# Kernel tuning notes

Measured on AMD Instinct MI355X. Metric: run time of the kernel, lower is better.

## Reference

```python
import jax, jax.numpy as jnp
import numpy as np

# Config matching init_kwargs: dim=256, input_resolution=(64,64), num_heads=8,
# stride=2, dynamic_factor=2, window_size=8, Attention_Group=2, postype='rel', k=None
DIM, H, W = 256, 64, 64
HEADS, HG, STRIDE, WS, FACTOR = 8, 2, 2, 8, 2.0
GC = DIM // HG                 # channels per attention group (offset net width)
HC = DIM // HEADS              # per-head channels
RH, RW = H // STRIDE, W // STRIDE
WH, WW = H // WS, W // WS
B = 2
MLP_HID = 4 * DIM
EPS = 1e-5


def _grid_sample(img, grid):
    # img: (N, C, H, W); grid: (N, Hg, Wg, 2) with (row, col) in [-1, 1].
    # Bilinear, align_corners=True, zero padding (matches F.grid_sample).
    N, C, Hi, Wi = img.shape
    rows = (grid[..., 0] + 1.0) * 0.5 * (Hi - 1)
    cols = (grid[..., 1] + 1.0) * 0.5 * (Wi - 1)
    r0f = jnp.floor(rows); c0f = jnp.floor(cols)
    wr = rows - r0f; wc = cols - c0f
    r0 = r0f.astype(jnp.int32); c0 = c0f.astype(jnp.int32)

    def gather(ri, ci):
        valid = ((ri >= 0) & (ri < Hi) & (ci >= 0) & (ci < Wi)).astype(img.dtype)
        rc = jnp.clip(ri, 0, Hi - 1); cc = jnp.clip(ci, 0, Wi - 1)
        vals = jax.vmap(lambda im, r, c: im[:, r, c])(img, rc, cc)  # (N, C, Hg, Wg)
        return vals * valid[:, None]

    return (gather(r0, c0) * ((1 - wr) * (1 - wc))[:, None]
            + gather(r0, c0 + 1) * ((1 - wr) * wc)[:, None]
            + gather(r0 + 1, c0) * (wr * (1 - wc))[:, None]
            + gather(r0 + 1, c0 + 1) * (wr * wc)[:, None])


def _ln2d(z, g, b):
    mu = jnp.mean(z, axis=1, keepdims=True)
    var = jnp.var(z, axis=1, keepdims=True)
    return (z - mu) * jax.lax.rsqrt(var + EPS) * g[None, :, None, None] + b[None, :, None, None]


def _conv1x1(z, w, b=None):
    out = jnp.einsum('oc,bchw->bohw', w, z)
    return out if b is None else out + b[None, :, None, None]


def _forward(x, ln1_g, ln1_b, q_w, q_b, k_w, k_b, v_w, v_b,
             off1_w, off2_w, off3_w, bn_g, bn_b, bn_m, bn_v, off4_w,
             posembed, proj_w, proj_b, ln2_g, ln2_b,
             mlp_w1, mlp_b1, mlp_w2, mlp_b2):
    Bx, C = x.shape[0], x.shape[1]
    R, NW, WT = RH * RW, WH * WW, WS * WS
    scale = C ** -0.5  # original uses dim**-0.5 (not head_dim) as default qk scale

    xa = _ln2d(x, ln1_g, ln1_b)
    q = _conv1x1(xa, q_w, q_b)

    # ---- per-group offset prediction: 3 depthwise strided convs -> BN -> GELU -> 1x1 ----
    qg = q.reshape(Bx * HG, GC, H, W)

    def dw(z, w):
        return jax.lax.conv_general_dilated(z, w, (2, 2), ((1, 1), (1, 1)),
                feature_group_count=GC, dimension_numbers=('NCHW', 'OIHW', 'NCHW'))

    o = dw(dw(dw(qg, off1_w), off2_w), off3_w)  # (B*HG, GC, WH, WW)
    o = (o - bn_m[None, :, None, None]) * jax.lax.rsqrt(bn_v + EPS)[None, :, None, None]
    o = o * bn_g[None, :, None, None] + bn_b[None, :, None, None]
    o = jax.nn.gelu(o, approximate=False)
    off = jnp.einsum('oc,bchw->bohw', off4_w, o)               # (B*HG, 2R, WH, WW)
    off = off.reshape(Bx * HG, 2, R, NW).transpose(0, 3, 2, 1)  # (B*HG, NW, R, 2)
    ranges = jnp.array([1.0 / H, 1.0 / W], dtype=x.dtype)
    off = jnp.tanh(off) * ranges * FACTOR

    # ---- reference points normalized to [-1, 1] (align_corners=True convention) ----
    ref_r = (jnp.arange(RH, dtype=x.dtype) * STRIDE) / (H - 1) * 2.0 - 1.0
    ref_c = (jnp.arange(RW, dtype=x.dtype) * STRIDE) / (W - 1) * 2.0 - 1.0
    ref = jnp.stack(jnp.meshgrid(ref_r, ref_c, indexing='ij'), axis=-1).reshape(R, 2)
    grid = off + ref[None, None]                                # (B*HG, NW, R, 2)

    # ---- deformable gather of values at predicted sample locations ----
    value = xa.reshape(Bx * HG, GC, H, W)
    samp = _grid_sample(value, grid).reshape(Bx, C, NW, R)

    kk = _conv1x1(samp, k_w, k_b).reshape(Bx * HEADS, HC, NW, R).transpose(0, 2, 1, 3)
    vv = _conv1x1(samp, v_w, v_b).reshape(Bx * HEADS, HC, NW, R).transpose(0, 2, 1, 3)

    # ---- windowed queries ----
    wq = q.reshape(Bx * HEADS, HC, H, W).transpose(0, 2, 3, 1)
    wq = wq.reshape(Bx * HEADS, WH, WS, WW, WS, HC).transpose(0, 1, 3, 2, 4, 5)
    wq = wq.reshape(Bx * HEADS, NW, WT, HC) * scale

    attn = jnp.einsum('nwqc,nwcr->nwqr', wq, kk)                # (B*h, NW, WT, R)

    # ---- relative position bias: query pixel vs. (stride-spaced) reference point ----
    rel_y = (jnp.arange(RH) * STRIDE)[None, :] - jnp.arange(H)[:, None] + (H - 1)  # (H, RH)
    rel_x = (jnp.arange(RW) * STRIDE)[None, :] - jnp.arange(W)[:, None] + (W - 1)  # (W, RW)
    t = posembed[:, rel_y, :]                                   # (h, H, RH, 2W-1)
    bias = t[:, :, :, rel_x]                                    # (h, H, RH, W, RW)
    bias = bias.transpose(0, 1, 3, 2, 4).reshape(HEADS, H, W, R)
    bias = bias.reshape(HEADS, WH, WS, WW, WS, R).transpose(0, 1, 3, 2, 4, 5)
    bias = bias.reshape(HEADS, NW, WT, R)

    attn = attn.reshape(Bx, HEADS, NW, WT, R) + bias[None]
    attn = jax.nn.softmax(attn, axis=-1).reshape(Bx * HEADS, NW, WT, R)
    out = jnp.einsum('nwqr,nwcr->nwqc', attn, vv)               # (B*h, NW, WT, HC)
    out = out.reshape(Bx * HEADS, WH, WW, WS, WS, HC).transpose(0, 1, 3, 2, 4, 5)
    out = out.reshape(Bx, HEADS, H, W, HC).transpose(0, 1, 4, 2, 3).reshape(Bx, C, H, W)
    out = _conv1x1(out, proj_w, proj_b)

    x = x + out
    xm = _ln2d(x, ln2_g, ln2_b)
    hdn = jax.nn.gelu(_conv1x1(xm, mlp_w1, mlp_b1), approximate=False)
    return x + _conv1x1(hdn, mlp_w2, mlp_b2)


def setup_inputs() -> dict:
    key = jax.random.key(0)
    ks = jax.random.split(key, 16)
    f32 = jnp.float32

    def n(k, shape, std=0.02):
        return jax.random.normal(k, shape, dtype=f32) * std

    R = RH * RW
    return {
        'x': jax.random.normal(ks[0], (B, DIM, H, W), dtype=f32),
        'ln1_g': jnp.ones((DIM,), f32), 'ln1_b': jnp.zeros((DIM,), f32),
        'q_w': n(ks[1], (DIM, DIM)), 'q_b': jnp.zeros((DIM,), f32),
        'k_w': n(ks[2], (DIM, DIM)), 'k_b': jnp.zeros((DIM,), f32),
        'v_w': n(ks[3], (DIM, DIM)), 'v_b': jnp.zeros((DIM,), f32),
        'off1_w': n(ks[4], (GC, 1, 3, 3)),
        'off2_w': n(ks[5], (GC, 1, 3, 3)),
        'off3_w': n(ks[6], (GC, 1, 3, 3)),
        'bn_g': jnp.ones((GC,), f32), 'bn_b': jnp.zeros((GC,), f32),
        'bn_m': jnp.zeros((GC,), f32), 'bn_v': jnp.ones((GC,), f32),
        'off4_w': n(ks[7], (2 * R, GC)),
        'posembed': n(ks[8], (HEADS, 2 * H - 1, 2 * W - 1), std=0.01),
        'proj_w': n(ks[9], (DIM, DIM)), 'proj_b': jnp.zeros((DIM,), f32),
        'ln2_g': jnp.ones((DIM,), f32), 'ln2_b': jnp.zeros((DIM,), f32),
        'mlp_w1': n(ks[10], (MLP_HID, DIM)), 'mlp_b1': jnp.zeros((MLP_HID,), f32),
        'mlp_w2': n(ks[11], (DIM, MLP_HID)), 'mlp_b2': jnp.zeros((DIM,), f32),
    }


def reference(x, ln1_g, ln1_b, q_w, q_b, k_w, k_b, v_w, v_b,
              off1_w, off2_w, off3_w, bn_g, bn_b, bn_m, bn_v, off4_w,
              posembed, proj_w, proj_b, ln2_g, ln2_b,
              mlp_w1, mlp_b1, mlp_w2, mlp_b2):
    return _forward(x, ln1_g, ln1_b, q_w, q_b, k_w, k_b, v_w, v_b,
                    off1_w, off2_w, off3_w, bn_g, bn_b, bn_m, bn_v, off4_w,
                    posembed, proj_w, proj_b, ln2_g, ln2_b,
                    mlp_w1, mlp_b1, mlp_w2, mlp_b2)
```

## Files before the change

### kernel.cpp

```cpp
#include <hip/hip_runtime.h>
#include <hip/hip_bf16.h>
#include <math.h>


typedef __hip_bfloat16 bf16;
typedef __bf16 bf16x8 __attribute__((ext_vector_type(8)));
typedef float f32x4 __attribute__((ext_vector_type(4)));
typedef unsigned int u32x4 __attribute__((ext_vector_type(4)));

union U16x8 { uint4 u4; u32x4 v4; unsigned short us[8]; };

__device__ __forceinline__ float cvt(float x) { return x; }
__device__ __forceinline__ float cvt(bf16 x) { return __bfloat162float(x); }
__device__ __forceinline__ float b2f(unsigned short u) {
  union { float f; unsigned int v; } x; x.v = ((unsigned int)u) << 16; return x.f;
}
__device__ __forceinline__ unsigned short f2b(float f) {
  bf16 h = __float2bfloat16(f);
  return *reinterpret_cast<unsigned short*>(&h);
}
__device__ __forceinline__ float gelu_f(float x) {
  return 0.5f * x * (1.0f + erff(x * 0.7071067811865475f));
}
__device__ __forceinline__ void stout(float* p, float v) { *p = v; }
__device__ __forceinline__ void stout(bf16* p, float v) { *p = __float2bfloat16(v); }

__global__ __launch_bounds__(256) void setup_kernel(
    const float* __restrict__ x, const float* __restrict__ g,
    const float* __restrict__ bta,
    const float* __restrict__ q_w, const float* __restrict__ q_b,
    const float* __restrict__ k_w, const float* __restrict__ v_w,
    const float* __restrict__ pjw, const float* __restrict__ w1,
    const float* __restrict__ w2, const float* __restrict__ off4w,
    bf16* __restrict__ out, float* __restrict__ xnhwc,
    unsigned short* __restrict__ wqkv, float* __restrict__ bqkv,
    unsigned short* __restrict__ wproj, unsigned short* __restrict__ wmlp1,
    unsigned short* __restrict__ wmlp2, unsigned short* __restrict__ woff4i)
{
  __shared__ float s1[8][32], s2[8][32];
  __shared__ unsigned short tb[32][264];
  int bid = blockIdx.x;
  int t = threadIdx.x;
  if (bid < 256) {
    int pos = t & 31, cs = t >> 5;
    int p = bid * 32 + pos;
    int bb = p >> 12, hw = p & 4095;
    const float* xp = x + (size_t)bb * 256 * 4096 + hw;
    float vloc[32];
    float sum = 0.f, ss = 0.f;
#pragma unroll
    for (int i = 0; i < 32; ++i) {
      float v = xp[(size_t)(cs * 32 + i) * 4096];
      vloc[i] = v; sum += v; ss += v * v;
    }
    s1[cs][pos] = sum; s2[cs][pos] = ss;
    {
      float* xo = xnhwc + (size_t)p * 256 + cs * 32;
#pragma unroll
      for (int qd = 0; qd < 8; ++qd)
        *(float4*)(xo + qd * 4) = make_float4(vloc[qd*4], vloc[qd*4+1],
                                              vloc[qd*4+2], vloc[qd*4+3]);
    }
    __syncthreads();
    if (cs == 0) {
      float S = 0.f, Q = 0.f;
#pragma unroll
      for (int i = 0; i < 8; ++i) { S += s1[i][pos]; Q += s2[i][pos]; }
      float mu = S * (1.f / 256.f);
      float var = Q * (1.f / 256.f) - mu * mu;
      s1[0][pos] = mu;
      s2[0][pos] = rsqrtf(var + 1e-5f);
    }
    __syncthreads();
    float mu = s1[0][pos], rs = s2[0][pos];
#pragma unroll
    for (int i = 0; i < 32; ++i) {
      int c = cs * 32 + i;
      tb[pos][c] = f2b((vloc[i] - mu) * rs * g[c] + bta[c]);
    }
    __syncthreads();
    int px = t >> 3, grp = t & 7;
    bf16* op = out + ((size_t)bid * 32 + px) * 256 + grp * 32;
#pragma unroll
    for (int q = 0; q < 4; ++q)
      *(uint4*)(op + q * 8) = *(const uint4*)&tb[px][grp * 32 + q * 8];
  } else {
    int idx = (bid - 256) * 256 + t;
    const int S0 = 768 * 256;
    const int S1 = S0 + 768;
    const int S2 = S1 + 256 * 256;
    const int S3 = S2 + 1024 * 256;
    const int S4 = S3 + 256 * 1024;
    const int S5 = S4 + 2048 * 128;
    if (idx < S0) {
      int n = idx >> 8, c = idx & 255;
      float v;
      if (n < 256)       v = q_w[n * 256 + c];
      else if (n < 512)  v = k_w[(n - 256) * 256 + c];
      else               v = v_w[(n - 512) * 256 + c];
      wqkv[idx] = f2b(v);
    } else if (idx < S1) {
      int n = idx - S0;
      bqkv[n] = (n < 256) ? q_b[n] : 0.f;
    } else if (idx < S2) {
      wproj[idx - S1] = f2b(pjw[idx - S1]);
    } else if (idx < S3) {
      wmlp1[idx - S2] = f2b(w1[idx - S2]);
    } else if (idx < S4) {
      wmlp2[idx - S3] = f2b(w2[idx - S3]);
    } else if (idx < S5) {
      int kk = idx - S4;
      int n = kk >> 7, c = kk & 127;
      woff4i[kk] = f2b(off4w[((size_t)((n & 1) * 1024 + (n >> 1))) * 128 + c]);
    }
  }
}

__global__ __launch_bounds__(256) void ln2_kernel(
    const bf16* __restrict__ xin, const float* __restrict__ g,
    const float* __restrict__ bta, bf16* __restrict__ out)
{
  __shared__ float sa[8][32], sb[8][32];
  __shared__ float mu_s[32], rs_s[32];
  int t = threadIdx.x;
  int px = t >> 3, grp = t & 7;
  size_t p = (size_t)blockIdx.x * 32 + px;
  const bf16* xp = xin + p * 256 + grp * 32;
  float v[32]; float sum = 0.f, ss = 0.f;
#pragma unroll
  for (int q = 0; q < 4; ++q) {
    U16x8 u; u.u4 = *(const uint4*)(xp + q * 8);
#pragma unroll
    for (int j = 0; j < 8; ++j) {
      float f = b2f(u.us[j]); v[q * 8 + j] = f; sum += f; ss += f * f;
    }
  }
  sa[grp][px] = sum; sb[grp][px] = ss;
  __syncthreads();
  if (t < 32) {
    float S = 0.f, Q = 0.f;
#pragma unroll
    for (int i = 0; i < 8; ++i) { S += sa[i][t]; Q += sb[i][t]; }
    float mu = S * (1.f / 256.f);
    mu_s[t] = mu;
    rs_s[t] = rsqrtf(Q * (1.f / 256.f) - mu * mu + 1e-5f);
  }
  __syncthreads();
  float mu = mu_s[px], rs = rs_s[px];
  bf16* op = out + p * 256 + grp * 32;
#pragma unroll
  for (int q = 0; q < 4; ++q) {
    U16x8 o;
#pragma unroll
    for (int j = 0; j < 8; ++j) {
      int c = grp * 32 + q * 8 + j;
      o.us[j] = f2b((v[q * 8 + j] - mu) * rs * g[c] + bta[c]);
    }
    *(uint4*)(op + q * 8) = o.u4;
  }
}

template<int OUTM, int RESM, int ACT, int BM>
__global__ __launch_bounds__(256) void mgemm_kernel(
    const bf16* __restrict__ A, const unsigned short* __restrict__ Bw,
    const float* __restrict__ bias, const void* __restrict__ res,
    void* __restrict__ out, int N, int K, int lda, int ldb)
{
  constexpr int MT = BM / 32;
  constexpr int AB_BYTES = (BM + 64) * 72 * 2;
  constexpr int T_LD = BM + 5;
  constexpr int T_BYTES = 64 * T_LD * 4;
  constexpr int SH_BYTES = (OUTM == 1 && T_BYTES > AB_BYTES) ? T_BYTES : AB_BYTES;
  __shared__ __attribute__((aligned(16))) char shraw[SH_BYTES];
  auto As = reinterpret_cast<unsigned short(*)[72]>(shraw);
  auto Bs = reinterpret_cast<unsigned short(*)[72]>(shraw + BM * 72 * 2);
  float (*T)[T_LD] = reinterpret_cast<float(*)[T_LD]>(shraw);

  int t = threadIdx.x;
  int m0 = blockIdx.y * BM, n0 = blockIdx.x * 64;
  int lane = t & 63, w = t >> 6;
  int l15 = lane & 15, quad = lane >> 4;
  int wm = (w >> 1) * (BM / 2), wn = (w & 1) * 32;
  f32x4 acc[MT][2];
#pragma unroll
  for (int mt = 0; mt < MT; ++mt)
#pragma unroll
    for (int nt = 0; nt < 2; ++nt) acc[mt][nt] = (f32x4){0.f, 0.f, 0.f, 0.f};

  for (int k0 = 0; k0 < K; k0 += 64) {
#pragma unroll
    for (int i = 0; i < MT; ++i) {
      int idx = t + i * 256;
      int m = idx >> 3, oc = (idx & 7) * 8;
      *(uint4*)&As[m][oc] = *(const uint4*)(A + (size_t)(m0 + m) * lda + k0 + oc);
    }
#pragma unroll
    for (int i = 0; i < 2; ++i) {
      int idx = t + i * 256;
      int n = idx >> 3, oc = (idx & 7) * 8;
      *(uint4*)&Bs[n][oc] = *(const uint4*)(Bw + (size_t)(n0 + n) * ldb + k0 + oc);
    }
    __syncthreads();
#pragma unroll
    for (int ks = 0; ks < 2; ++ks) {
      bf16x8 af[MT], bfr[2];
#pragma unroll
      for (int mt = 0; mt < MT; ++mt)
        af[mt] = __builtin_bit_cast(bf16x8,
            *(const uint4*)&As[wm + mt * 16 + l15][ks * 32 + quad * 8]);
#pragma unroll
      for (int nt = 0; nt < 2; ++nt)
        bfr[nt] = __builtin_bit_cast(bf16x8,
            *(const uint4*)&Bs[wn + nt * 16 + l15][ks * 32 + quad * 8]);
#pragma unroll
      for (int mt = 0; mt < MT; ++mt)
#pragma unroll
        for (int nt = 0; nt < 2; ++nt)
          acc[mt][nt] = __builtin_amdgcn_mfma_f32_16x16x32_bf16(
              af[mt], bfr[nt], acc[mt][nt], 0, 0, 0);
    }
    __syncthreads();
  }
  float bv[2];
#pragma unroll
  for (int nt = 0; nt < 2; ++nt)
    bv[nt] = bias ? bias[n0 + wn + nt * 16 + l15] : 0.f;
#pragma unroll
  for (int mt = 0; mt < MT; ++mt) {
#pragma unroll
    for (int nt = 0; nt < 2; ++nt) {
#pragma unroll
      for (int reg = 0; reg < 4; ++reg) {
        int m = m0 + wm + mt * 16 + quad * 4 + reg;
        int n = n0 + wn + nt * 16 + l15;
        float v = acc[mt][nt][reg] + bv[nt];
        if constexpr (ACT == 1) v = gelu_f(v);
        if constexpr (RESM == 1)
          v += ((const float*)res)[(size_t)m * N + n];
        if constexpr (RESM == 2)
          v += b2f(((const unsigned short*)res)[(size_t)m * N + n]);
        if constexpr (OUTM == 0)
          ((unsigned short*)out)[(size_t)m * N + n] = f2b(v);
        if constexpr (OUTM == 1)
          T[(n - n0)][(m - m0)] = v;
        if constexpr (OUTM == 4)
          ((unsigned short*)out)[((size_t)(n >> 8) * 8192 + m) * 256 + (n & 255)] = f2b(v);
        if constexpr (OUTM == 5) {
          float val = tanhf(v) * (2.0f / 64.0f);
          int r = n >> 1, coord = n & 1;
          int rc = coord ? (r & 31) : (r >> 5);
          float ref = rc * (4.0f / 63.0f) - 1.0f;
          float pix = (val + ref + 1.0f) * 31.5f;
          float other = __shfl_xor(pix, 1, 64);
          if (coord == 0) {
            float rowp = pix, colp = other;
            float r0f = floorf(rowp), c0f = floorf(colp);
            float wr = rowp - r0f, wc = colp - c0f;
            int r0 = (int)r0f, c0 = (int)c0f;
            bool rv0 = ((unsigned)r0 < 64u), rv1 = ((unsigned)(r0 + 1) < 64u);
            bool cv0 = ((unsigned)c0 < 64u), cv1 = ((unsigned)(c0 + 1) < 64u);
            float4 w4;
            w4.x = (rv0 && cv0) ? (1.f - wr) * (1.f - wc) : 0.f;
            w4.y = (rv0 && cv1) ? (1.f - wr) * wc : 0.f;
            w4.z = (rv1 && cv0) ? wr * (1.f - wc) : 0.f;
            w4.w = (rv1 && cv1) ? wr * wc : 0.f;
            ((int*)out)[(size_t)m * 1024 + r] = r0 * 64 + c0;
            *(float4*)((float*)res + ((size_t)m * 1024 + r) * 4) = w4;
          }
        }
      }
    }
  }
  if constexpr (OUTM == 1) {
    __syncthreads();
    constexpr int SEGS = BM / 32;
    int units = 64 * SEGS;
    if (t < units) {
      int nl = t / SEGS, seg = t % SEGS;
      int bI = m0 >> 12, hw0 = m0 & 4095;
      float* op = (float*)out + ((size_t)bI * 256 + n0 + nl) * 4096 + hw0 + seg * 32;
#pragma unroll
      for (int k = 0; k < 32; ++k) op[k] = T[nl][seg * 32 + k];
    }
  }
}

template<typename TI, typename TO, int IC>
__global__ __launch_bounds__(256) void dwconv_kernel(
    const TI* __restrict__ in, const float* __restrict__ wgt,
    TO* __restrict__ out, int Hi, int Wi, int Ho, int Wo, int fuse,
    const float* __restrict__ bg_, const float* __restrict__ bb_,
    const float* __restrict__ bm_, const float* __restrict__ bv_)
{
  int idx = blockIdx.x * 256 + threadIdx.x;
  int c = idx & 127;
  int pp = idx >> 7;
  int ow = pp % Wo, oh = (pp / Wo) % Ho, bgi = pp / (Wo * Ho);
  const TI* ip;
  if constexpr (IC == 256)
    ip = in + ((size_t)(bgi >> 1) * 4096) * 256 + (bgi & 1) * 128 + c;
  else
    ip = in + ((size_t)bgi * Hi * Wi) * 128 + c;
  float acc = 0.f;
#pragma unroll
  for (int ky = 0; ky < 3; ++ky) {
    int ih = oh * 2 - 1 + ky;
    if ((unsigned)ih >= (unsigned)Hi) continue;
#pragma unroll
    for (int kx = 0; kx < 3; ++kx) {
      int iw = ow * 2 - 1 + kx;
      if ((unsigned)iw >= (unsigned)Wi) continue;
      acc += wgt[c * 9 + ky * 3 + kx] * cvt(ip[(size_t)(ih * Wi + iw) * IC]);
    }
  }
  if (fuse) {
    acc = (acc - bm_[c]) * rsqrtf(bv_[c] + 1e-5f) * bg_[c] + bb_[c];
    acc = gelu_f(acc);
  }
  stout(out + idx, acc);
}

__global__ __launch_bounds__(256) void gatherkv_kernel(
    const unsigned short* __restrict__ Kimg, const unsigned short* __restrict__ Vimg,
    const int* __restrict__ goff, const float* __restrict__ gwt,
    unsigned short* __restrict__ Ks, unsigned short* __restrict__ Vs)
{
  int t = threadIdx.x;
  int pos = blockIdx.x * 8 + (t >> 5);
  int oct = t & 31;
  int r = pos & 1023;
  int nw = (pos >> 10) & 63;
  int b = pos >> 16;
  int ch0 = oct * 8;
  int g = oct >> 4;

  size_t cbase = ((size_t)(b * 2 + g) * 64 + nw) * 1024 + r;
  int base = goff[cbase];
  f32x4 wv = *(const f32x4*)(gwt + cbase * 4);
  int o00 = min(max(base, 0), 4095);
  int o01 = min(max(base + 1, 0), 4095);
  int o10 = min(max(base + 64, 0), 4095);
  int o11 = min(max(base + 65, 0), 4095);
  size_t pb = ((size_t)b * 4096) * 256 + ch0;
  uint4 kc[4], vc[4];
  kc[0] = *(const uint4*)(Kimg + pb + (size_t)o00 * 256);
  kc[1] = *(const uint4*)(Kimg + pb + (size_t)o01 * 256);
  kc[2] = *(const uint4*)(Kimg + pb + (size_t)o10 * 256);
  kc[3] = *(const uint4*)(Kimg + pb + (size_t)o11 * 256);
  vc[0] = *(const uint4*)(Vimg + pb + (size_t)o00 * 256);
  vc[1] = *(const uint4*)(Vimg + pb + (size_t)o01 * 256);
  vc[2] = *(const uint4*)(Vimg + pb + (size_t)o10 * 256);
  vc[3] = *(const uint4*)(Vimg + pb + (size_t)o11 * 256);

  float aK[8] = {0.f,0.f,0.f,0.f,0.f,0.f,0.f,0.f};
  float aV[8] = {0.f,0.f,0.f,0.f,0.f,0.f,0.f,0.f};
#pragma unroll
  for (int c4 = 0; c4 < 4; ++c4) {
    U16x8 ku, vu; ku.u4 = kc[c4]; vu.u4 = vc[c4];
    float wvv = wv[c4];
#pragma unroll
    for (int j = 0; j < 8; ++j) {
      aK[j] += wvv * b2f(ku.us[j]);
      aV[j] += wvv * b2f(vu.us[j]);
    }
  }
  U16x8 ok, ov;
#pragma unroll
  for (int j = 0; j < 8; ++j) { ok.us[j] = f2b(aK[j]); ov.us[j] = f2b(aV[j]); }
  int head = oct >> 2, chh = (oct & 3) * 8;
  size_t obase = (((size_t)(b * 8 + head) * 64 + nw) * 1024 + r) * 32 + chh;
  __builtin_nontemporal_store(ok.v4, (u32x4*)(Ks + obase));
  __builtin_nontemporal_store(ov.v4, (u32x4*)(Vs + obase));
}

__global__ __launch_bounds__(256) void attn2_kernel(
    const bf16* __restrict__ qbuf, const unsigned short* __restrict__ Ks,
    const unsigned short* __restrict__ Vs, const float* __restrict__ vbv,
    const float* __restrict__ pe, bf16* __restrict__ aout)
{
  __shared__ unsigned short vs[2][32][72];
  __shared__ unsigned short PsQs[64][72];
  __shared__ unsigned short pesb[70][72];

  const float LOG2E = 1.4426950408889634f;
  int blk = blockIdx.x;
  int b = blk & 1, head = (blk >> 1) & 7, nw = blk >> 4;
  int wh = nw >> 3, ww = nw & 7;
  int t = threadIdx.x;
  int lane = t & 63, w = t >> 6;
  int l15 = lane & 15, quad = lane >> 4;
  int qc0 = head * 32;
  int vr = t >> 2, vseg = t & 3;

  size_t kvbase = ((size_t)(b * 8 + head) * 64 + nw) * 32768;
  const unsigned short* Kb = Ks + kvbase;
  const unsigned short* Vb = Vs + kvbase;

  {
    int qt = t >> 2, oct = t & 3;
    int h = wh * 8 + (qt >> 3), wcol = ww * 8 + (qt & 7);
    const bf16* src = qbuf + ((size_t)b * 4096 + h * 64 + wcol) * 256 + qc0 + oct * 8;
    U16x8 u; u.u4 = *(const uint4*)src;
    U16x8 o;
#pragma unroll
    for (int j = 0; j < 8; ++j) o.us[j] = f2b(b2f(u.us[j]) * (0.0625f * LOG2E));
    *(uint4*)&PsQs[qt][oct * 8] = o.u4;
  }
  int ry0 = 56 - wh * 8, rx0 = 56 - ww * 8;
  for (int i = t; i < 70 * 70; i += 256) {
    int yy = i / 70, xx = i % 70;
    pesb[yy][xx] = f2b(pe[(size_t)head * 16129 + (ry0 + yy) * 127 + rx0 + xx] * LOG2E);
  }
  {
    U16x8 vu; vu.u4 = *(const uint4*)(Vb + (size_t)t * 8);
#pragma unroll
    for (int j = 0; j < 8; ++j) {
      int row = vseg * 8 + j;
      vs[0][row][vr ^ (((row >> 3) & 3) * 8)] = vu.us[j];
    }
  }
  uint4 kf[4];
#pragma unroll
  for (int nt = 0; nt < 4; ++nt)
    kf[nt] = *(const uint4*)(Kb + (size_t)(nt * 16 + l15) * 32 + quad * 8);
  __syncthreads();

  bf16x8 aQ = __builtin_bit_cast(bf16x8, *(const uint4*)&PsQs[w * 16 + l15][quad * 8]);
  float l[4] = {0.f, 0.f, 0.f, 0.f};
  f32x4 oacc[2];
  oacc[0] = (f32x4){0.f, 0.f, 0.f, 0.f};
  oacc[1] = (f32x4){0.f, 0.f, 0.f, 0.f};

  uint4 vcn = make_uint4(0u, 0u, 0u, 0u);
  uint4 kfn[4];
  for (int c = 0; c < 16; ++c) {
    int cur = c & 1, rc0 = c * 64;
    if (c) {
      U16x8 vu; vu.u4 = vcn;
#pragma unroll
      for (int j = 0; j < 8; ++j) {
        int row = vseg * 8 + j;
        vs[cur][row][vr ^ (((row >> 3) & 3) * 8)] = vu.us[j];
      }
      __syncthreads();
    }
    if (c < 15) {
      size_t nb = (size_t)(rc0 + 64) * 32;
      vcn = *(const uint4*)(Vb + nb + (size_t)t * 8);
#pragma unroll
      for (int nt = 0; nt < 4; ++nt)
        kfn[nt] = *(const uint4*)(Kb + nb + (size_t)(nt * 16 + l15) * 32 + quad * 8);
    }

    f32x4 s[4];
#pragma unroll
    for (int nt = 0; nt < 4; ++nt) {
      bf16x8 bK = __builtin_bit_cast(bf16x8, kf[nt]);
      f32x4 z = (f32x4){0.f, 0.f, 0.f, 0.f};
      s[nt] = __builtin_amdgcn_mfma_f32_16x16x32_bf16(aQ, bK, z, 0, 0, 0);
    }
#pragma unroll
    for (int nt = 0; nt < 4; ++nt) {
      int rg_ = nt * 16 + l15;
      int rrow = (rc0 + rg_) >> 5, rcol = rg_ & 31;
#pragma unroll
      for (int reg = 0; reg < 4; ++reg) {
        int q = w * 16 + quad * 4 + reg;
        s[nt][reg] += b2f(pesb[2 * rrow + 7 - (q >> 3)][2 * rcol + 7 - (q & 7)]);
      }
    }
#pragma unroll
    for (int reg = 0; reg < 4; ++reg) {
      float ps = 0.f;
#pragma unroll
      for (int nt = 0; nt < 4; ++nt) {
        float p = exp2f(s[nt][reg]);
        PsQs[w * 16 + quad * 4 + reg][nt * 16 + l15] = f2b(p);
        ps += p;
      }
      l[reg] += ps;
    }
#pragma unroll
    for (int kst = 0; kst < 2; ++kst) {
      uint4 up = *(const uint4*)&PsQs[w * 16 + l15][kst * 32 + quad * 8];
      bf16x8 pA = __builtin_bit_cast(bf16x8, up);
#pragma unroll
      for (int nt2 = 0; nt2 < 2; ++nt2) {
        int row = nt2 * 16 + l15;
        int cbase = (kst * 32 + quad * 8) ^ (((row >> 3) & 3) * 8);
        uint4 uv = *(const uint4*)&vs[cur][row][cbase];
        bf16x8 vB = __builtin_bit_cast(bf16x8, uv);
        oacc[nt2] = __builtin_amdgcn_mfma_f32_16x16x32_bf16(pA, vB, oacc[nt2], 0, 0, 0);
      }
    }
    if (c < 15) {
#pragma unroll
      for (int nt = 0; nt < 4; ++nt) kf[nt] = kfn[nt];
    }
  }
#pragma unroll
  for (int reg = 0; reg < 4; ++reg) {
    l[reg] += __shfl_xor(l[reg], 1, 64);
    l[reg] += __shfl_xor(l[reg], 2, 64);
    l[reg] += __shfl_xor(l[reg], 4, 64);
    l[reg] += __shfl_xor(l[reg], 8, 64);
  }
#pragma unroll
  for (int nt2 = 0; nt2 < 2; ++nt2) {
    float vbias = vbv[qc0 + nt2 * 16 + l15];
#pragma unroll
    for (int reg = 0; reg < 4; ++reg) {
      int q = w * 16 + quad * 4 + reg;
      size_t p = (size_t)b * 4096 + (wh * 8 + (q >> 3)) * 64 + ww * 8 + (q & 7);
      aout[p * 256 + qc0 + nt2 * 16 + l15] =
          __float2bfloat16(oacc[nt2][reg] / l[reg] + vbias);
    }
  }
}

extern "C" void kernel_launch(void* const* d_in, const int* in_sizes, int n_in,
                              void* d_out, int out_size, void* d_ws, size_t ws_size,
                              hipStream_t stream) {
  (void)in_sizes; (void)n_in; (void)out_size; (void)ws_size;
  const float* x     = (const float*)d_in[0];
  const float* ln1g  = (const float*)d_in[1];
  const float* ln1b  = (const float*)d_in[2];
  const float* q_w   = (const float*)d_in[3];
  const float* q_b   = (const float*)d_in[4];
  const float* k_w   = (const float*)d_in[5];
  const float* k_b   = (const float*)d_in[6];
  const float* v_w   = (const float*)d_in[7];
  const float* v_b   = (const float*)d_in[8];
  const float* off1w = (const float*)d_in[9];
  const float* off2w = (const float*)d_in[10];
  const float* off3w = (const float*)d_in[11];
  const float* bng   = (const float*)d_in[12];
  const float* bnb   = (const float*)d_in[13];
  const float* bnm   = (const float*)d_in[14];
  const float* bnv   = (const float*)d_in[15];
  const float* off4w = (const float*)d_in[16];
  const float* pe    = (const float*)d_in[17];
  const float* pjw   = (const float*)d_in[18];
  const float* pjb   = (const float*)d_in[19];
  const float* ln2g  = (const float*)d_in[20];
  const float* ln2b  = (const float*)d_in[21];
  const float* w1    = (const float*)d_in[22];
  const float* b1    = (const float*)d_in[23];
  const float* w2    = (const float*)d_in[24];
  const float* b2    = (const float*)d_in[25];
  (void)k_b;
  float* outp = (float*)d_out;

  char* W = (char*)d_ws;
  bf16*  xa    = (bf16*) (W + 0);
  float* dw1   = (float*)(W + 8388608);
  float* dw2   = (float*)(W + 10485760);
  bf16*  dw3b  = (bf16*) (W + 11010048);
  bf16*  qkv   = (bf16*) (W + 13238272);
  bf16*  qb    = qkv;
  bf16*  Kimg  = qkv + 2097152;
  bf16*  Vimg  = qkv + 2 * 2097152;
  bf16*  x2    = (bf16*) (W + 34209792);
  float* xnhwc = (float*)(W + 38404096);
  unsigned short* wqkv   = (unsigned short*)(W + 46792704);
  float*          bqkv   = (float*)         (W + 47448064);
  unsigned short* wproj  = (unsigned short*)(W + 47453184);
  unsigned short* wmlp1  = (unsigned short*)(W + 47584256);
  unsigned short* wmlp2  = (unsigned short*)(W + 48108544);
  unsigned short* woff4i = (unsigned short*)(W + 48632832);
  int*   goff  = (int*)  (W + 49157120);
  float* gwt   = (float*)(W + 50205696);
  unsigned short* Ksmp = (unsigned short*)(W + 54525952);
  unsigned short* Vsmp = (unsigned short*)(W + 121634816);
  bf16*  aout = xa;
  bf16*  xm   = xa;
  bf16*  hdn  = Kimg;

  setup_kernel<<<4356, 256, 0, stream>>>(
      x, ln1g, ln1b, q_w, q_b, k_w, v_w, pjw, w1, w2, off4w,
      xa, xnhwc, wqkv, bqkv, wproj, wmlp1, wmlp2, woff4i);
  mgemm_kernel<4, 0, 0, 128><<<dim3(12, 64), 256, 0, stream>>>(
      xa, wqkv, bqkv, nullptr, qkv, 768, 256, 256, 256);
  dwconv_kernel<bf16, float, 256><<<2048, 256, 0, stream>>>(
      qb, off1w, dw1, 64, 64, 32, 32, 0, nullptr, nullptr, nullptr, nullptr);
  dwconv_kernel<float, float, 128><<<512, 256, 0, stream>>>(
      dw1, off2w, dw2, 32, 32, 16, 16, 0, nullptr, nullptr, nullptr, nullptr);
  dwconv_kernel<float, bf16, 128><<<128, 256, 0, stream>>>(
      dw2, off3w, dw3b, 16, 16, 8, 8, 1, bng, bnb, bnm, bnv);
  mgemm_kernel<5, 0, 0, 64><<<dim3(32, 4), 256, 0, stream>>>(
      dw3b, woff4i, nullptr, (const void*)gwt, goff, 2048, 128, 128, 128);
  gatherkv_kernel<<<16384, 256, 0, stream>>>(
      (const unsigned short*)Kimg, (const unsigned short*)Vimg,
      goff, gwt, Ksmp, Vsmp);
  attn2_kernel<<<1024, 256, 0, stream>>>(
      qb, Ksmp, Vsmp, v_b, pe, aout);
  mgemm_kernel<0, 1, 0, 64><<<dim3(4, 128), 256, 0, stream>>>(
      aout, wproj, pjb, (const void*)xnhwc, x2, 256, 256, 256, 256);
  ln2_kernel<<<256, 256, 0, stream>>>(x2, ln2g, ln2b, xm);
  mgemm_kernel<0, 0, 1, 128><<<dim3(16, 64), 256, 0, stream>>>(
      xm, wmlp1, b1, nullptr, hdn, 1024, 256, 256, 256);
  mgemm_kernel<1, 2, 0, 64><<<dim3(4, 128), 256, 0, stream>>>(
      hdn, wmlp2, b2, (const void*)x2, outp, 256, 1024, 1024, 1024);
}
```

Measured before the change: 276.3 us.

## Parameterize GEMM N-tile, widen tiles, vectorize pos-bias loads, add MFMA setprio

New measurement: 278.9 us. About the same (+0.9%).

```diff
diff --git a/kernel.cpp b/kernel.cpp
--- a/kernel.cpp
+++ b/kernel.cpp
@@ -9,11 +9,18 @@
 typedef unsigned int u32x4 __attribute__((ext_vector_type(4)));
 
 union U16x8 { uint4 u4; u32x4 v4; unsigned short us[8]; };
+union FU { float f; unsigned int u; };
 
 __device__ __forceinline__ float cvt(float x) { return x; }
 __device__ __forceinline__ float cvt(bf16 x) { return __bfloat162float(x); }
 __device__ __forceinline__ float b2f(unsigned short u) {
   union { float f; unsigned int v; } x; x.v = ((unsigned int)u) << 16; return x.f;
+}
+__device__ __forceinline__ float hi2f(unsigned int u) {
+  FU x; x.u = u & 0xffff0000u; return x.f;
+}
+__device__ __forceinline__ float lo2f(unsigned int u) {
+  FU x; x.u = u << 16; return x.f;
 }
 __device__ __forceinline__ unsigned short f2b(float f) {
   bf16 h = __float2bfloat16(f);
@@ -160,14 +167,15 @@
   }
 }
 
-template<int OUTM, int RESM, int ACT, int BM>
+template<int OUTM, int RESM, int ACT, int BM, int BN>
 __global__ __launch_bounds__(256) void mgemm_kernel(
     const bf16* __restrict__ A, const unsigned short* __restrict__ Bw,
     const float* __restrict__ bias, const void* __restrict__ res,
     void* __restrict__ out, int N, int K, int lda, int ldb)
 {
   constexpr int MT = BM / 32;
-  constexpr int AB_BYTES = (BM + 64) * 72 * 2;
+  constexpr int WNT = BN / 32;
+  constexpr int AB_BYTES = (BM + BN) * 72 * 2;
   constexpr int T_LD = BM + 5;
   constexpr int T_BYTES = 64 * T_LD * 4;
   constexpr int SH_BYTES = (OUTM == 1 && T_BYTES > AB_BYTES) ? T_BYTES : AB_BYTES;
@@ -177,15 +185,15 @@
   float (*T)[T_LD] = reinterpret_cast<float(*)[T_LD]>(shraw);
 
   int t = threadIdx.x;
-  int m0 = blockIdx.y * BM, n0 = blockIdx.x * 64;
+  int m0 = blockIdx.y * BM, n0 = blockIdx.x * BN;
   int lane = t & 63, w = t >> 6;
   int l15 = lane & 15, quad = lane >> 4;
-  int wm = (w >> 1) * (BM / 2), wn = (w & 1) * 32;
-  f32x4 acc[MT][2];
+  int wm = (w >> 1) * (BM / 2), wn = (w & 1) * (BN / 2);
+  f32x4 acc[MT][WNT];
 #pragma unroll
   for (int mt = 0; mt < MT; ++mt)
 #pragma unroll
-    for (int nt = 0; nt < 2; ++nt) acc[mt][nt] = (f32x4){0.f, 0.f, 0.f, 0.f};
+    for (int nt = 0; nt < WNT; ++nt) acc[mt][nt] = (f32x4){0.f, 0.f, 0.f, 0.f};
 
   for (int k0 = 0; k0 < K; k0 += 64) {
 #pragma unroll
@@ -195,7 +203,7 @@
       *(uint4*)&As[m][oc] = *(const uint4*)(A + (size_t)(m0 + m) * lda + k0 + oc);
     }
 #pragma unroll
-    for (int i = 0; i < 2; ++i) {
+    for (int i = 0; i < WNT; ++i) {
       int idx = t + i * 256;
       int n = idx >> 3, oc = (idx & 7) * 8;
       *(uint4*)&Bs[n][oc] = *(const uint4*)(Bw + (size_t)(n0 + n) * ldb + k0 + oc);
@@ -203,32 +211,32 @@
     __syncthreads();
 #pragma unroll
     for (int ks = 0; ks < 2; ++ks) {
-      bf16x8 af[MT], bfr[2];
+      bf16x8 af[MT], bfr[WNT];
 #pragma unroll
       for (int mt = 0; mt < MT; ++mt)
         af[mt] = __builtin_bit_cast(bf16x8,
             *(const uint4*)&As[wm + mt * 16 + l15][ks * 32 + quad * 8]);
 #pragma unroll
-      for (int nt = 0; nt < 2; ++nt)
+      for (int nt = 0; nt < WNT; ++nt)
         bfr[nt] = __builtin_bit_cast(bf16x8,
             *(const uint4*)&Bs[wn + nt * 16 + l15][ks * 32 + quad * 8]);
 #pragma unroll
       for (int mt = 0; mt < MT; ++mt)
 #pragma unroll
-        for (int nt = 0; nt < 2; ++nt)
+        for (int nt = 0; nt < WNT; ++nt)
           acc[mt][nt] = __builtin_amdgcn_mfma_f32_16x16x32_bf16(
               af[mt], bfr[nt], acc[mt][nt], 0, 0, 0);
     }
     __syncthreads();
   }
-  float bv[2];
-#pragma unroll
-  for (int nt = 0; nt < 2; ++nt)
+  float bv[WNT];
+#pragma unroll
+  for (int nt = 0; nt < WNT; ++nt)
     bv[nt] = bias ? bias[n0 + wn + nt * 16 + l15] : 0.f;
 #pragma unroll
   for (int mt = 0; mt < MT; ++mt) {
 #pragma unroll
-    for (int nt = 0; nt < 2; ++nt) {
+    for (int nt = 0; nt < WNT; ++nt) {
 #pragma unroll
       for (int reg = 0; reg < 4; ++reg) {
         int m = m0 + wm + mt * 16 + quad * 4 + reg;
@@ -431,10 +439,13 @@
   oacc[0] = (f32x4){0.f, 0.f, 0.f, 0.f};
   oacc[1] = (f32x4){0.f, 0.f, 0.f, 0.f};
 
+  int rowbase = 7 - (w * 2 + (quad >> 1));
+  int Cb = 2 * l15 + 7 - (quad & 1) * 4;
+
   uint4 vcn = make_uint4(0u, 0u, 0u, 0u);
   uint4 kfn[4];
   for (int c = 0; c < 16; ++c) {
-    int cur = c & 1, rc0 = c * 64;
+    int cur = c & 1;
     if (c) {
       U16x8 vu; vu.u4 = vcn;
 #pragma unroll
@@ -445,7 +456,7 @@
       __syncthreads();
     }
     if (c < 15) {
-      size_t nb = (size_t)(rc0 + 64) * 32;
+      size_t nb = (size_t)(c * 64 + 64) * 32;
       vcn = *(const uint4*)(Vb + nb + (size_t)t * 8);
 #pragma unroll
       for (int nt = 0; nt < 4; ++nt)
@@ -453,21 +464,25 @@
     }
 
     f32x4 s[4];
+    __builtin_amdgcn_s_setprio(1);
 #pragma unroll
     for (int nt = 0; nt < 4; ++nt) {
       bf16x8 bK = __builtin_bit_cast(bf16x8, kf[nt]);
       f32x4 z = (f32x4){0.f, 0.f, 0.f, 0.f};
       s[nt] = __builtin_amdgcn_mfma_f32_16x16x32_bf16(aQ, bK, z, 0, 0, 0);
     }
+    __builtin_amdgcn_s_setprio(0);
 #pragma unroll
     for (int nt = 0; nt < 4; ++nt) {
-      int rg_ = nt * 16 + l15;
-      int rrow = (rc0 + rg_) >> 5, rcol = rg_ & 31;
-#pragma unroll
-      for (int reg = 0; reg < 4; ++reg) {
-        int q = w * 16 + quad * 4 + reg;
-        s[nt][reg] += b2f(pesb[2 * rrow + 7 - (q >> 3)][2 * rcol + 7 - (q & 7)]);
-      }
+      int row = rowbase + 4 * c + 2 * (nt >> 1);
+      int C = Cb + (nt & 1) * 32;
+      const unsigned int* pr = (const unsigned int*)&pesb[row][0];
+      unsigned int pa = pr[(C - 3) >> 1];
+      unsigned int pbm = pr[(C - 1) >> 1];
+      s[nt][0] += hi2f(pbm);
+      s[nt][1] += lo2f(pbm);
+      s[nt][2] += hi2f(pa);
+      s[nt][3] += lo2f(pa);
     }
 #pragma unroll
     for (int reg = 0; reg < 4; ++reg) {
@@ -480,6 +495,7 @@
       }
       l[reg] += ps;
     }
+    __builtin_amdgcn_s_setprio(1);
 #pragma unroll
     for (int kst = 0; kst < 2; ++kst) {
       uint4 up = *(const uint4*)&PsQs[w * 16 + l15][kst * 32 + quad * 8];
@@ -493,6 +509,7 @@
         oacc[nt2] = __builtin_amdgcn_mfma_f32_16x16x32_bf16(pA, vB, oacc[nt2], 0, 0, 0);
       }
     }
+    __builtin_amdgcn_s_setprio(0);
     if (c < 15) {
 #pragma unroll
       for (int nt = 0; nt < 4; ++nt) kf[nt] = kfn[nt];
@@ -579,7 +596,7 @@
   setup_kernel<<<4356, 256, 0, stream>>>(
       x, ln1g, ln1b, q_w, q_b, k_w, v_w, pjw, w1, w2, off4w,
       xa, xnhwc, wqkv, bqkv, wproj, wmlp1, wmlp2, woff4i);
-  mgemm_kernel<4, 0, 0, 128><<<dim3(12, 64), 256, 0, stream>>>(
+  mgemm_kernel<4, 0, 0, 128, 128><<<dim3(6, 64), 256, 0, stream>>>(
       xa, wqkv, bqkv, nullptr, qkv, 768, 256, 256, 256);
   dwconv_kernel<bf16, float, 256><<<2048, 256, 0, stream>>>(
       qb, off1w, dw1, 64, 64, 32, 32, 0, nullptr, nullptr, nullptr, nullptr);
@@ -587,18 +604,18 @@
       dw1, off2w, dw2, 32, 32, 16, 16, 0, nullptr, nullptr, nullptr, nullptr);
   dwconv_kernel<float, bf16, 128><<<128, 256, 0, stream>>>(
       dw2, off3w, dw3b, 16, 16, 8, 8, 1, bng, bnb, bnm, bnv);
-  mgemm_kernel<5, 0, 0, 64><<<dim3(32, 4), 256, 0, stream>>>(
+  mgemm_kernel<5, 0, 0, 64, 64><<<dim3(32, 4), 256, 0, stream>>>(
       dw3b, woff4i, nullptr, (const void*)gwt, goff, 2048, 128, 128, 128);
   gatherkv_kernel<<<16384, 256, 0, stream>>>(
       (const unsigned short*)Kimg, (const unsigned short*)Vimg,
       goff, gwt, Ksmp, Vsmp);
   attn2_kernel<<<1024, 256, 0, stream>>>(
       qb, Ksmp, Vsmp, v_b, pe, aout);
-  mgemm_kernel<0, 1, 0, 64><<<dim3(4, 128), 256, 0, stream>>>(
+  mgemm_kernel<0, 1, 0, 64, 128><<<dim3(2, 128), 256, 0, stream>>>(
       aout, wproj, pjb, (const void*)xnhwc, x2, 256, 256, 256, 256);
   ln2_kernel<<<256, 256, 0, stream>>>(x2, ln2g, ln2b, xm);
-  mgemm_kernel<0, 0, 1, 128><<<dim3(16, 64), 256, 0, stream>>>(
+  mgemm_kernel<0, 0, 1, 128, 128><<<dim3(8, 64), 256, 0, stream>>>(
       xm, wmlp1, b1, nullptr, hdn, 1024, 256, 256, 256);
-  mgemm_kernel<1, 2, 0, 64><<<dim3(4, 128), 256, 0, stream>>>(
+  mgemm_kernel<1, 2, 0, 64, 64><<<dim3(4, 128), 256, 0, stream>>>(
       hdn, wmlp2, b2, (const void*)x2, outp, 256, 1024, 1024, 1024);
 }
```
